# Kernel tuning notes

Hardware: AMD Instinct MI355X
Metric: run time of the kernel (lower is better)

## Reference

```python
import jax, jax.numpy as jnp
import numpy as np

NUM_ROUTERS = 8
K = 2
IN_DIM = 384
HID = 64
TEMP = 1.0
AUX_COEF = 0.05
EPS = 1e-12


def _l2norm(v, axis=-1):
    n = jnp.sqrt(jnp.sum(v * v, axis=axis, keepdims=True))
    return v / jnp.maximum(n, EPS)


def setup_inputs() -> dict:
    key = jax.random.key(0)
    ks = jax.random.split(key, 10)
    B, E = 8192, 1024
    s = 1.0 / np.sqrt(IN_DIM)
    return {
        "x": jax.random.normal(ks[0], (B, IN_DIM), jnp.float32),
        "reasoning_embeddings": jax.random.normal(ks[1], (E, IN_DIM), jnp.float32),
        "random_num": jax.random.uniform(ks[2], (B, 1), jnp.float32),
        "gate_w": jax.random.normal(ks[3], (IN_DIM, NUM_ROUTERS), jnp.float32) * s,
        "gate_b": jnp.zeros((NUM_ROUTERS,), jnp.float32),
        "Uw": jax.random.normal(ks[4], (NUM_ROUTERS, IN_DIM, HID), jnp.float32) * s,
        "Ub": jnp.zeros((NUM_ROUTERS, HID), jnp.float32),
        "Vw": jax.random.normal(ks[5], (NUM_ROUTERS, IN_DIM, HID), jnp.float32) * s,
        "Vb": jnp.zeros((NUM_ROUTERS, HID), jnp.float32),
    }


def reference(x, reasoning_embeddings, random_num, gate_w, gate_b, Uw, Ub, Vw, Vb):
    B = x.shape[0]
    # gate
    logits = x @ gate_w + gate_b                              # [B, R]
    probs = jax.nn.softmax(logits, axis=-1)
    topk_vals, topk_idxs = jax.lax.top_k(logits, K)           # [B, K]
    topk_mask = jax.nn.one_hot(topk_idxs, NUM_ROUTERS).sum(axis=1)  # [B, R]
    aux_loss = NUM_ROUTERS * (probs.mean(0) * topk_mask.mean(0)).sum() * AUX_COEF

    # all routers, batched (replaces the per-(i,j) python loop)
    xu = _l2norm(jnp.einsum("bd,rdh->rbh", x, Uw) + Ub[:, None, :])          # [R, B, H]
    ev = _l2norm(jnp.einsum("ed,rdh->reh", reasoning_embeddings, Vw) + Vb[:, None, :])  # [R, E, H]
    scores = jnp.einsum("rbh,reh->rbe", xu, ev)               # [R, B, E]
    all_out = jax.nn.softmax(scores / TEMP, axis=-1)          # [R, B, E]

    # gather top-k experts per sample
    all_out_b = jnp.transpose(all_out, (1, 0, 2))             # [B, R, E]
    router_outputs = jnp.take_along_axis(all_out_b, topk_idxs[:, :, None], axis=1)  # [B, K, E]

    gate_weights = jax.nn.softmax(topk_vals, axis=-1)[:, :, None]  # [B, K, 1]
    rea_probs = jnp.sum(router_outputs * gate_weights, axis=1)     # [B, E]

    # categorical sampling via inverse-CDF
    scores_cumsum = jnp.cumsum(rea_probs, axis=1)
    selected_index = jnp.argmax((scores_cumsum > random_num).astype(jnp.float32), axis=1)  # [B]
    log_probs = jnp.log(rea_probs[jnp.arange(B), selected_index])[:, None]  # [B, 1]
    return selected_index, log_probs, aux_loss
```

## Files before the change

kernel.cpp:

```cpp
#include <hip/hip_runtime.h>
#include <math.h>

#define B 8192
#define E 1024
#define D 384
#define H 64
#define R 8
#define NCHUNK 16
#define CHUNK_E 64

#define WS_COUNTS   0u
#define WS_CURSORS  32u
#define WS_PS       64u
#define WS_TOP2     256u
#define WS_GW       65792u
#define WS_LIST     131328u
#define WS_EVN      196864u
#define WS_XUN      2294016u
#define WS_C        6488320u
#define WS_POSMAP   7536896u

__global__ __launch_bounds__(256) void k_gate(
    const float* __restrict__ x, const float* __restrict__ gate_w,
    const float* __restrict__ gate_b, int2* __restrict__ top2,
    float2* __restrict__ gwv, int* __restrict__ counts, float* __restrict__ ps)
{
  __shared__ __align__(16) float gwT[R * 388];
  __shared__ float psl[R];
  __shared__ int   cl[R];
  int tid = threadIdx.x;
  for (int idx = tid; idx < D * R; idx += 256) {
    int k = idx >> 3, r = idx & 7;
    gwT[r * 388 + k] = gate_w[idx];
  }
  if (tid < R) { psl[tid] = 0.f; cl[tid] = 0; }
  __syncthreads();

  int l = tid & 63;
  int r = tid & 7;
  int b = blockIdx.x * 32 + (tid >> 3);
  float acc = gate_b[r];
  const float4* x4 = (const float4*)(x + (size_t)b * D);
  const float*  gr = gwT + r * 388;
#pragma unroll 4
  for (int q = 0; q < 96; ++q) {
    float4 xv = x4[q];
    float4 gv = *(const float4*)&gr[q * 4];
    acc = fmaf(xv.x, gv.x, acc);
    acc = fmaf(xv.y, gv.y, acc);
    acc = fmaf(xv.z, gv.z, acc);
    acc = fmaf(xv.w, gv.w, acc);
  }
  float lv[R];
#pragma unroll
  for (int rr = 0; rr < R; ++rr) lv[rr] = __shfl(acc, (l & ~7) + rr);
  int i0 = 0; float v0 = lv[0];
#pragma unroll
  for (int rr = 1; rr < R; ++rr) if (lv[rr] > v0) { v0 = lv[rr]; i0 = rr; }
  int i1 = (i0 == 0) ? 1 : 0; float v1 = lv[i1];
#pragma unroll
  for (int rr = 0; rr < R; ++rr)
    if (rr != i0 && lv[rr] > v1) { v1 = lv[rr]; i1 = rr; }
  float se = 0.f;
#pragma unroll
  for (int rr = 0; rr < R; ++rr) se += expf(lv[rr] - v0);
  float p = expf(acc - v0) / se;
  if (r == 0) {
    float e10 = expf(v1 - v0);
    top2[b] = make_int2(i0, i1);
    gwv[b]  = make_float2(1.f / (1.f + e10), e10 / (1.f + e10));
  }
  float pa = p;
  int   ca = (r == i0 ? 1 : 0) + (r == i1 ? 1 : 0);
#pragma unroll
  for (int m = 8; m < 64; m <<= 1) {
    pa += __shfl_xor(pa, m);
    ca += __shfl_xor(ca, m);
  }
  if (l < 8) { atomicAdd(&psl[r], pa); atomicAdd(&cl[r], ca); }
  __syncthreads();
  if (tid < R) { atomicAdd(&ps[tid], psl[tid]); atomicAdd(&counts[tid], cl[tid]); }
}

__global__ __launch_bounds__(256) void k_scatter(
    const int2* __restrict__ top2, const int* __restrict__ counts,
    const float* __restrict__ ps, int* __restrict__ cursors,
    int* __restrict__ list, int2* __restrict__ posmap, float* __restrict__ out_aux)
{
  __shared__ int lc[R];
  __shared__ int lbase[R];
  __shared__ int offs[R];
  int tid = threadIdx.x;
  if (tid < R) { lc[tid] = 0; offs[tid] = min(counts[tid], B); }
  __syncthreads();
  if (tid == 0) {
    int o = 0;
    for (int r2 = 0; r2 < R; ++r2) { int c = offs[r2]; offs[r2] = o; o += c; }
  }
  __syncthreads();
  int b = min(blockIdx.x * 256 + tid, B - 1);
  int2 t = top2[b];
  t.x &= 7; t.y &= 7;
  int p0 = atomicAdd(&lc[t.x], 1);
  int p1 = atomicAdd(&lc[t.y], 1);
  __syncthreads();
  if (tid < R) lbase[tid] = atomicAdd(&cursors[tid], lc[tid]);
  __syncthreads();
  int i0 = min(offs[t.x] + lbase[t.x] + p0, 2 * B - 1);
  int i1 = min(offs[t.y] + lbase[t.y] + p1, 2 * B - 1);
  list[i0] = b * 2 + 0;
  list[i1] = b * 2 + 1;
  posmap[b] = make_int2(i0, i1);
  if (blockIdx.x == 0 && tid == 0) {
    float s = 0.f;
    for (int r2 = 0; r2 < R; ++r2)
      s += (ps[r2] / (float)B) * ((float)min(counts[r2], B) / (float)B);
    out_aux[0] = (float)R * s * 0.05f;
  }
}

__global__ __launch_bounds__(128) void k_proj(
    const float* __restrict__ re, const float* __restrict__ x,
    const float* __restrict__ Vw, const float* __restrict__ Vb,
    const float* __restrict__ Uw, const float* __restrict__ Ub,
    const int* __restrict__ list, const int* __restrict__ counts,
    float* __restrict__ evnT, float* __restrict__ xunP)
{
  __shared__ __align__(16) float At[64 * 32];
  __shared__ __align__(16) float Wt[64 * 64];
  __shared__ int cntL[R];
  int tid = threadIdx.x;
  int bid = blockIdx.x;
  if (tid < R) cntL[tid] = min(counts[tid], B);
  __syncthreads();

  bool isE = (bid < 256);
  int r, row0, n, base = 0;
  const float* Wsrc; const float* bias;
  if (isE) {
    r = bid >> 5; row0 = (bid & 31) * 32; n = 32;
    Wsrc = Vw + (size_t)r * D * H; bias = Vb + r * H;
  } else {
    int idx = bid - 256;
    r = idx >> 8; row0 = (idx & 255) * 32;
    int cnt = cntL[r];
    if (row0 >= cnt) return;
    n = min(32, cnt - row0);
    for (int rr = 0; rr < r; ++rr) base += cntL[rr];
    base += row0;
    Wsrc = Uw + (size_t)r * D * H; bias = Ub + r * H;
  }

  int rowS = tid & 31, kq = tid >> 5;
  const float4* Arow;
  if (isE) {
    Arow = (const float4*)re + (size_t)(row0 + rowS) * 96;
  } else {
    int g = list[min(base + min(rowS, n - 1), 2 * B - 1)] & (2 * B - 1);
    Arow = (const float4*)x + (size_t)(g >> 1) * 96;
  }
  const float4* W4 = (const float4*)Wsrc;

  int rg = tid >> 4;
  int hg = tid & 15;
  float4 bv = *(const float4*)(bias + hg * 4);
  float acc[4][4];
#pragma unroll
  for (int i = 0; i < 4; ++i) {
    acc[i][0] = bv.x; acc[i][1] = bv.y; acc[i][2] = bv.z; acc[i][3] = bv.w;
  }

  for (int kt = 0; kt < 6; ++kt) {
    __syncthreads();
#pragma unroll
    for (int q = 0; q < 4; ++q) {
      float4 v = Arow[kt * 16 + kq + 4 * q];
      int kb = (kq + 4 * q) * 4;
      At[(kb + 0) * 32 + rowS] = v.x;
      At[(kb + 1) * 32 + rowS] = v.y;
      At[(kb + 2) * 32 + rowS] = v.z;
      At[(kb + 3) * 32 + rowS] = v.w;
    }
#pragma unroll
    for (int q = 0; q < 8; ++q) {
      int idx2 = tid + 128 * q;
      int k = idx2 >> 4, h4 = idx2 & 15;
      *(float4*)&Wt[k * 64 + h4 * 4] = W4[(size_t)(kt * 64 + k) * 16 + h4];
    }
    __syncthreads();
#pragma unroll 8
    for (int k = 0; k < 64; ++k) {
      float4 a4 = *(const float4*)&At[k * 32 + rg * 4];
      float4 w4 = *(const float4*)&Wt[k * 64 + hg * 4];
      const float* ap = (const float*)&a4;
      const float* wp = (const float*)&w4;
#pragma unroll
      for (int i = 0; i < 4; ++i)
#pragma unroll
        for (int j = 0; j < 4; ++j) acc[i][j] = fmaf(ap[i], wp[j], acc[i][j]);
    }
  }

  float rn[4];
#pragma unroll
  for (int i = 0; i < 4; ++i) {
    float ss = 0.f;
#pragma unroll
    for (int j = 0; j < 4; ++j) ss = fmaf(acc[i][j], acc[i][j], ss);
#pragma unroll
    for (int m = 1; m < 16; m <<= 1) ss += __shfl_xor(ss, m);
    rn[i] = 1.f / fmaxf(sqrtf(ss), 1e-12f);
  }

  if (isE) {
#pragma unroll
    for (int j = 0; j < 4; ++j) {
      float4 o;
      o.x = acc[0][j] * rn[0]; o.y = acc[1][j] * rn[1];
      o.z = acc[2][j] * rn[2]; o.w = acc[3][j] * rn[3];
      *(float4*)(evnT + (size_t)(r * 64 + hg * 4 + j) * 1024 + row0 + rg * 4) = o;
    }
  } else {
#pragma unroll
    for (int i = 0; i < 4; ++i) {
      int row = rg * 4 + i;
      if (row < n) {
        float4 o;
        o.x = acc[i][0] * rn[i]; o.y = acc[i][1] * rn[i];
        o.z = acc[i][2] * rn[i]; o.w = acc[i][3] * rn[i];
        *(float4*)(xunP + (size_t)(base + row) * H + hg * 4) = o;
      }
    }
  }
}

__global__ __launch_bounds__(256) void k_pass1(
    const float* __restrict__ evnT, const float* __restrict__ xunP,
    const int* __restrict__ counts, float* __restrict__ C)
{
  __shared__ __align__(16) float Xt[64 * 128];
  __shared__ __align__(16) float Et[64 * 64];
  __shared__ int cntL[R];
  int tid = threadIdx.x;
  if (tid < R) cntL[tid] = min(counts[tid], B);
  __syncthreads();

  int bid = blockIdx.x;
  int et    = bid & 15;
  int stile = (bid >> 4) & 63;
  int r     = bid >> 10;
  int cnt = cntL[r];
  if (cnt <= 0 || stile * 128 >= cnt) return;
  int off = 0;
  for (int rr = 0; rr < r; ++rr) off += cntL[rr];
  off += stile * 128;
  int n = min(128, cnt - stile * 128);
  int ebase = et * 64;

  {
    int row = tid >> 1;
    int rc  = min(row, n - 1);
    const float4* src = (const float4*)(xunP + (size_t)(off + rc) * H);
    int hq0 = (tid & 1) * 8;
#pragma unroll
    for (int q = 0; q < 8; ++q) {
      float4 v = src[hq0 + q];
      int h = (hq0 + q) * 4;
      Xt[(h + 0) * 128 + row] = v.x;
      Xt[(h + 1) * 128 + row] = v.y;
      Xt[(h + 2) * 128 + row] = v.z;
      Xt[(h + 3) * 128 + row] = v.w;
    }
  }
  {
#pragma unroll
    for (int q = 0; q < 4; ++q) {
      int idx = tid + 256 * q;
      int h = idx >> 4, e4 = idx & 15;
      float4 v = *(const float4*)(evnT + (size_t)(r * 64 + h) * 1024 + ebase + e4 * 4);
      *(float4*)&Et[h * 64 + e4 * 4] = v;
    }
  }
  __syncthreads();

  int sg = tid >> 4, egr = tid & 15;
  float acc[8][4];
#pragma unroll
  for (int i = 0; i < 8; ++i)
#pragma unroll
    for (int j = 0; j < 4; ++j) acc[i][j] = 0.f;

#pragma unroll 4
  for (int k = 0; k < 64; ++k) {
    float4 xa = *(const float4*)&Xt[k * 128 + sg * 8];
    float4 xb = *(const float4*)&Xt[k * 128 + sg * 8 + 4];
    float4 ev = *(const float4*)&Et[k * 64 + egr * 4];
    const float* ep = (const float*)&ev;
    const float* pa = (const float*)&xa;
    const float* pb = (const float*)&xb;
#pragma unroll
    for (int i = 0; i < 4; ++i)
#pragma unroll
      for (int j = 0; j < 4; ++j) {
        acc[i][j]     = fmaf(pa[i], ep[j], acc[i][j]);
        acc[i + 4][j] = fmaf(pb[i], ep[j], acc[i + 4][j]);
      }
  }

#pragma unroll
  for (int i = 0; i < 8; ++i) {
    float v = expf(acc[i][0]) + expf(acc[i][1]) + expf(acc[i][2]) + expf(acc[i][3]);
#pragma unroll
    for (int m = 1; m < 16; m <<= 1) v += __shfl_xor(v, m);
    int s = sg * 8 + i;
    if (egr == 0 && s < n) C[(size_t)(off + s) * NCHUNK + et] = v;
  }
}

__global__ __launch_bounds__(256) void k_pass2(
    const float* __restrict__ evnT, const float* __restrict__ xunP,
    const float* __restrict__ C, const int2* __restrict__ top2,
    const int2* __restrict__ posmap, const float2* __restrict__ gwv,
    const float* __restrict__ rnd, float* __restrict__ out)
{
  int tid = threadIdx.x;
  int lane = tid & 63;
  int b = blockIdx.x * 4 + (tid >> 6);
  if (b >= B) return;
  int2 t2 = top2[b];
  t2.x &= 7; t2.y &= 7;
  int2 pm = posmap[b];
  pm.x &= (2 * B - 1); pm.y &= (2 * B - 1);
  float2 gw = gwv[b];
  float rv = rnd[b];

  const float4* C04 = (const float4*)(C + (size_t)pm.x * NCHUNK);
  const float4* C14 = (const float4*)(C + (size_t)pm.y * NCHUNK);
  float c0[NCHUNK], c1[NCHUNK];
#pragma unroll
  for (int q = 0; q < 4; ++q) {
    float4 v0 = C04[q], v1 = C14[q];
    c0[q*4+0]=v0.x; c0[q*4+1]=v0.y; c0[q*4+2]=v0.z; c0[q*4+3]=v0.w;
    c1[q*4+0]=v1.x; c1[q*4+1]=v1.y; c1[q*4+2]=v1.z; c1[q*4+3]=v1.w;
  }
  float S0 = 0.f, S1 = 0.f;
#pragma unroll
  for (int j = 0; j < NCHUNK; ++j) { S0 += c0[j]; S1 += c1[j]; }
  float a0 = gw.x / S0, a1 = gw.y / S1;
  int cstar = -1; float prefix = 0.f; float run = 0.f;
#pragma unroll
  for (int j = 0; j < NCHUNK; ++j) {
    float nrun = run + (c0[j] * a0 + c1[j] * a1);
    if (cstar < 0 && nrun > rv) { cstar = j; prefix = run; }
    run = nrun;
  }
  float rtgt = rv;
  if (cstar < 0) { cstar = 0; prefix = 0.f; rtgt = -1.0f; }

  float xu0 = xunP[(size_t)pm.x * H + lane];
  float xu1 = xunP[(size_t)pm.y * H + lane];
  const float* E0 = evnT + (size_t)t2.x * 64 * 1024 + cstar * CHUNK_E + lane;
  const float* E1 = evnT + (size_t)t2.y * 64 * 1024 + cstar * CHUNK_E + lane;
  float d0 = 0.f, d1 = 0.f;
#pragma unroll 16
  for (int h = 0; h < 64; ++h) {
    float w0 = __shfl(xu0, h);
    float w1 = __shfl(xu1, h);
    d0 = fmaf(E0[(size_t)h * 1024], w0, d0);
    d1 = fmaf(E1[(size_t)h * 1024], w1, d1);
  }
  float rea = expf(d0) * a0 + expf(d1) * a1;
  float sc = rea;
#pragma unroll
  for (int d = 1; d < 64; d <<= 1) {
    float o = __shfl_up(sc, d);
    if (lane >= d) sc += o;
  }
  float cum = prefix + sc;
  unsigned long long m2 = __ballot(cum > rtgt);
  int estar = (m2 == 0ull) ? 63 : (int)__builtin_ctzll(m2);
  float p = __shfl(rea, estar);
  if (lane == 0) {
    int sel = cstar * CHUNK_E + estar;
    out[b]     = (float)sel;
    out[B + b] = logf(p);
  }
}

extern "C" void kernel_launch(void* const* d_in, const int* in_sizes, int n_in,
                              void* d_out, int out_size, void* d_ws, size_t ws_size,
                              hipStream_t stream)
{
  (void)in_sizes; (void)n_in; (void)out_size; (void)ws_size;
  const float* x      = (const float*)d_in[0];
  const float* re     = (const float*)d_in[1];
  const float* rnd    = (const float*)d_in[2];
  const float* gate_w = (const float*)d_in[3];
  const float* gate_b = (const float*)d_in[4];
  const float* Uw     = (const float*)d_in[5];
  const float* Ub     = (const float*)d_in[6];
  const float* Vw     = (const float*)d_in[7];
  const float* Vb     = (const float*)d_in[8];
  char* ws = (char*)d_ws;
  int*    counts  = (int*)(ws + WS_COUNTS);
  int*    cursors = (int*)(ws + WS_CURSORS);
  float*  ps      = (float*)(ws + WS_PS);
  int2*   top2    = (int2*)(ws + WS_TOP2);
  float2* gwv     = (float2*)(ws + WS_GW);
  int*    list    = (int*)(ws + WS_LIST);
  float*  evnT    = (float*)(ws + WS_EVN);
  float*  xunP    = (float*)(ws + WS_XUN);
  float*  Cc      = (float*)(ws + WS_C);
  int2*   posmap  = (int2*)(ws + WS_POSMAP);
  float* out = (float*)d_out;

  hipMemsetAsync(ws, 0, 256, stream);
  k_gate   <<<256,  256, 0, stream>>>(x, gate_w, gate_b, top2, gwv, counts, ps);
  k_scatter<<<32,   256, 0, stream>>>(top2, counts, ps, cursors, list, posmap, out + 2 * B);
  k_proj   <<<2304, 128, 0, stream>>>(re, x, Vw, Vb, Uw, Ub, list, counts, evnT, xunP);
  k_pass1  <<<8192, 256, 0, stream>>>(evnT, xunP, counts, Cc);
  k_pass2  <<<2048, 256, 0, stream>>>(evnT, xunP, Cc, top2, posmap, gwv, rnd, out);
}
```

Baseline: 184.7 us.

## Rewrite projection with wave-level readlane GEMM and widen pass1 E tiles

The projection kernel drops its shared-memory tiles. Each wave now computes 8 rows by 64 hidden units, holding weights in registers and broadcasting inputs with readlane, which removes LDS traffic and barriers. Pass1 doubles its E tile to 128 columns (8x8 accumulators per thread), halving the number of blocks and the reloads of each X tile. Router segment offsets are padded to multiples of 8 and the workspace is relaid out. The trade is higher register pressure and uncoalesced per-row weight loads in the projection.

```diff
diff --git a/kernel.cpp b/kernel.cpp
--- a/kernel.cpp
+++ b/kernel.cpp
@@ -8,17 +8,18 @@
 #define R 8
 #define NCHUNK 16
 #define CHUNK_E 64
+#define NPOS 16448
 
 #define WS_COUNTS   0u
 #define WS_CURSORS  32u
 #define WS_PS       64u
 #define WS_TOP2     256u
 #define WS_GW       65792u
-#define WS_LIST     131328u
-#define WS_EVN      196864u
-#define WS_XUN      2294016u
-#define WS_C        6488320u
-#define WS_POSMAP   7536896u
+#define WS_POSMAP   131328u
+#define WS_LIST     196864u
+#define WS_EVN      262656u
+#define WS_XUN      2359808u
+#define WS_C        6570496u
 
 __global__ __launch_bounds__(256) void k_gate(
     const float* __restrict__ x, const float* __restrict__ gate_w,
@@ -91,11 +92,11 @@
   __shared__ int lbase[R];
   __shared__ int offs[R];
   int tid = threadIdx.x;
-  if (tid < R) { lc[tid] = 0; offs[tid] = min(counts[tid], B); }
+  if (tid < R) lc[tid] = 0;
   __syncthreads();
   if (tid == 0) {
     int o = 0;
-    for (int r2 = 0; r2 < R; ++r2) { int c = offs[r2]; offs[r2] = o; o += c; }
+    for (int r2 = 0; r2 < R; ++r2) { offs[r2] = o; o += (min(counts[r2], B) + 7) & ~7; }
   }
   __syncthreads();
   int b = min(blockIdx.x * 256 + tid, B - 1);
@@ -106,8 +107,8 @@
   __syncthreads();
   if (tid < R) lbase[tid] = atomicAdd(&cursors[tid], lc[tid]);
   __syncthreads();
-  int i0 = min(offs[t.x] + lbase[t.x] + p0, 2 * B - 1);
-  int i1 = min(offs[t.y] + lbase[t.y] + p1, 2 * B - 1);
+  int i0 = min(offs[t.x] + lbase[t.x] + p0, NPOS - 1);
+  int i1 = min(offs[t.y] + lbase[t.y] + p1, NPOS - 1);
   list[i0] = b * 2 + 0;
   list[i1] = b * 2 + 1;
   posmap[b] = make_int2(i0, i1);
@@ -119,118 +120,96 @@
   }
 }
 
-__global__ __launch_bounds__(128) void k_proj(
+__global__ __launch_bounds__(256) void k_proj(
     const float* __restrict__ re, const float* __restrict__ x,
     const float* __restrict__ Vw, const float* __restrict__ Vb,
     const float* __restrict__ Uw, const float* __restrict__ Ub,
     const int* __restrict__ list, const int* __restrict__ counts,
     float* __restrict__ evnT, float* __restrict__ xunP)
 {
-  __shared__ __align__(16) float At[64 * 32];
-  __shared__ __align__(16) float Wt[64 * 64];
-  __shared__ int cntL[R];
   int tid = threadIdx.x;
+  int lane = tid & 63;
+  int wv = tid >> 6;
   int bid = blockIdx.x;
-  if (tid < R) cntL[tid] = min(counts[tid], B);
-  __syncthreads();
 
   bool isE = (bid < 256);
-  int r, row0, n, base = 0;
-  const float* Wsrc; const float* bias;
+  int r, g, n = 32, base = 0;
+  const float *W, *bias;
   if (isE) {
-    r = bid >> 5; row0 = (bid & 31) * 32; n = 32;
-    Wsrc = Vw + (size_t)r * D * H; bias = Vb + r * H;
+    r = bid >> 5; g = bid & 31;
+    W = Vw + (size_t)r * (D * H); bias = Vb + r * H;
   } else {
     int idx = bid - 256;
-    r = idx >> 8; row0 = (idx & 255) * 32;
-    int cnt = cntL[r];
-    if (row0 >= cnt) return;
-    n = min(32, cnt - row0);
-    for (int rr = 0; rr < r; ++rr) base += cntL[rr];
-    base += row0;
-    Wsrc = Uw + (size_t)r * D * H; bias = Ub + r * H;
-  }
-
-  int rowS = tid & 31, kq = tid >> 5;
-  const float4* Arow;
+    r = idx >> 8; g = idx & 255;
+    int cnt = min(counts[r], B);
+    if (g * 32 >= cnt) return;
+    n = min(32, cnt - g * 32);
+    for (int rr = 0; rr < r; ++rr) base += (min(counts[rr], B) + 7) & ~7;
+    base += g * 32;
+    W = Uw + (size_t)r * (D * H); bias = Ub + r * H;
+  }
+  int row0 = wv * 8;
+  if (row0 >= n) return;
+
+  const float* arow[8];
+#pragma unroll
+  for (int i = 0; i < 8; ++i) {
+    int rr = min(row0 + i, n - 1);
+    if (isE) {
+      arow[i] = re + (size_t)(g * 32 + rr) * D;
+    } else {
+      int gl = list[min(base + rr, NPOS - 1)];
+      gl = min(max(gl, 0), 2 * B - 1);
+      arow[i] = x + (size_t)(gl >> 1) * D;
+    }
+  }
+  float bv = bias[lane];
+  float acc[8];
+#pragma unroll
+  for (int i = 0; i < 8; ++i) acc[i] = bv;
+
+  for (int c = 0; c < 6; ++c) {
+    float w[64];
+#pragma unroll
+    for (int k = 0; k < 64; ++k) w[k] = W[(size_t)(c * 64 + k) * H + lane];
+    float xa[8];
+#pragma unroll
+    for (int i = 0; i < 8; ++i) xa[i] = arow[i][c * 64 + lane];
+#pragma unroll
+    for (int k = 0; k < 64; ++k) {
+      float wk = w[k];
+#pragma unroll
+      for (int i = 0; i < 8; ++i) {
+        float s = __uint_as_float(__builtin_amdgcn_readlane(__float_as_uint(xa[i]), k));
+        acc[i] = fmaf(s, wk, acc[i]);
+      }
+    }
+  }
+
+  float rn[8];
+#pragma unroll
+  for (int i = 0; i < 8; ++i) {
+    float ss = acc[i] * acc[i];
+#pragma unroll
+    for (int m = 1; m < 64; m <<= 1) ss += __shfl_xor(ss, m);
+    rn[i] = 1.f / fmaxf(sqrtf(ss), 1e-12f);
+  }
+
   if (isE) {
-    Arow = (const float4*)re + (size_t)(row0 + rowS) * 96;
+    int e0 = g * 32 + row0;
+    float4 o0, o1;
+    o0.x = acc[0] * rn[0]; o0.y = acc[1] * rn[1];
+    o0.z = acc[2] * rn[2]; o0.w = acc[3] * rn[3];
+    o1.x = acc[4] * rn[4]; o1.y = acc[5] * rn[5];
+    o1.z = acc[6] * rn[6]; o1.w = acc[7] * rn[7];
+    float* dst = evnT + (size_t)(r * 64 + lane) * 1024 + e0;
+    *(float4*)dst = o0;
+    *(float4*)(dst + 4) = o1;
   } else {
-    int g = list[min(base + min(rowS, n - 1), 2 * B - 1)] & (2 * B - 1);
-    Arow = (const float4*)x + (size_t)(g >> 1) * 96;
-  }
-  const float4* W4 = (const float4*)Wsrc;
-
-  int rg = tid >> 4;
-  int hg = tid & 15;
-  float4 bv = *(const float4*)(bias + hg * 4);
-  float acc[4][4];
-#pragma unroll
-  for (int i = 0; i < 4; ++i) {
-    acc[i][0] = bv.x; acc[i][1] = bv.y; acc[i][2] = bv.z; acc[i][3] = bv.w;
-  }
-
-  for (int kt = 0; kt < 6; ++kt) {
-    __syncthreads();
-#pragma unroll
-    for (int q = 0; q < 4; ++q) {
-      float4 v = Arow[kt * 16 + kq + 4 * q];
-      int kb = (kq + 4 * q) * 4;
-      At[(kb + 0) * 32 + rowS] = v.x;
-      At[(kb + 1) * 32 + rowS] = v.y;
-      At[(kb + 2) * 32 + rowS] = v.z;
-      At[(kb + 3) * 32 + rowS] = v.w;
-    }
-#pragma unroll
-    for (int q = 0; q < 8; ++q) {
-      int idx2 = tid + 128 * q;
-      int k = idx2 >> 4, h4 = idx2 & 15;
-      *(float4*)&Wt[k * 64 + h4 * 4] = W4[(size_t)(kt * 64 + k) * 16 + h4];
-    }
-    __syncthreads();
-#pragma unroll 8
-    for (int k = 0; k < 64; ++k) {
-      float4 a4 = *(const float4*)&At[k * 32 + rg * 4];
-      float4 w4 = *(const float4*)&Wt[k * 64 + hg * 4];
-      const float* ap = (const float*)&a4;
-      const float* wp = (const float*)&w4;
-#pragma unroll
-      for (int i = 0; i < 4; ++i)
-#pragma unroll
-        for (int j = 0; j < 4; ++j) acc[i][j] = fmaf(ap[i], wp[j], acc[i][j]);
-    }
-  }
-
-  float rn[4];
-#pragma unroll
-  for (int i = 0; i < 4; ++i) {
-    float ss = 0.f;
-#pragma unroll
-    for (int j = 0; j < 4; ++j) ss = fmaf(acc[i][j], acc[i][j], ss);
-#pragma unroll
-    for (int m = 1; m < 16; m <<= 1) ss += __shfl_xor(ss, m);
-    rn[i] = 1.f / fmaxf(sqrtf(ss), 1e-12f);
-  }
-
-  if (isE) {
-#pragma unroll
-    for (int j = 0; j < 4; ++j) {
-      float4 o;
-      o.x = acc[0][j] * rn[0]; o.y = acc[1][j] * rn[1];
-      o.z = acc[2][j] * rn[2]; o.w = acc[3][j] * rn[3];
-      *(float4*)(evnT + (size_t)(r * 64 + hg * 4 + j) * 1024 + row0 + rg * 4) = o;
-    }
-  } else {
-#pragma unroll
-    for (int i = 0; i < 4; ++i) {
-      int row = rg * 4 + i;
-      if (row < n) {
-        float4 o;
-        o.x = acc[i][0] * rn[i]; o.y = acc[i][1] * rn[i];
-        o.z = acc[i][2] * rn[i]; o.w = acc[i][3] * rn[i];
-        *(float4*)(xunP + (size_t)(base + row) * H + hg * 4) = o;
-      }
-    }
+#pragma unroll
+    for (int i = 0; i < 8; ++i)
+      if (row0 + i < n)
+        xunP[(size_t)(base + row0 + i) * H + lane] = acc[i] * rn[i];
   }
 }
 
@@ -239,23 +218,23 @@
     const int* __restrict__ counts, float* __restrict__ C)
 {
   __shared__ __align__(16) float Xt[64 * 128];
-  __shared__ __align__(16) float Et[64 * 64];
+  __shared__ __align__(16) float Et[64 * 128];
   __shared__ int cntL[R];
   int tid = threadIdx.x;
   if (tid < R) cntL[tid] = min(counts[tid], B);
   __syncthreads();
 
   int bid = blockIdx.x;
-  int et    = bid & 15;
-  int stile = (bid >> 4) & 63;
-  int r     = bid >> 10;
+  int et    = bid & 7;
+  int stile = (bid >> 3) & 63;
+  int r     = bid >> 9;
   int cnt = cntL[r];
   if (cnt <= 0 || stile * 128 >= cnt) return;
   int off = 0;
-  for (int rr = 0; rr < r; ++rr) off += cntL[rr];
+  for (int rr = 0; rr < r; ++rr) off += (cntL[rr] + 7) & ~7;
   off += stile * 128;
   int n = min(128, cnt - stile * 128);
-  int ebase = et * 64;
+  int ebase = et * 128;
 
   {
     int row = tid >> 1;
@@ -274,46 +253,57 @@
   }
   {
 #pragma unroll
-    for (int q = 0; q < 4; ++q) {
+    for (int q = 0; q < 8; ++q) {
       int idx = tid + 256 * q;
-      int h = idx >> 4, e4 = idx & 15;
+      int h = idx >> 5, e4 = idx & 31;
       float4 v = *(const float4*)(evnT + (size_t)(r * 64 + h) * 1024 + ebase + e4 * 4);
-      *(float4*)&Et[h * 64 + e4 * 4] = v;
+      *(float4*)&Et[h * 128 + e4 * 4] = v;
     }
   }
   __syncthreads();
 
   int sg = tid >> 4, egr = tid & 15;
-  float acc[8][4];
+  float acc[8][8];
 #pragma unroll
   for (int i = 0; i < 8; ++i)
 #pragma unroll
-    for (int j = 0; j < 4; ++j) acc[i][j] = 0.f;
+    for (int j = 0; j < 8; ++j) acc[i][j] = 0.f;
 
 #pragma unroll 4
   for (int k = 0; k < 64; ++k) {
     float4 xa = *(const float4*)&Xt[k * 128 + sg * 8];
     float4 xb = *(const float4*)&Xt[k * 128 + sg * 8 + 4];
-    float4 ev = *(const float4*)&Et[k * 64 + egr * 4];
-    const float* ep = (const float*)&ev;
+    float4 ea = *(const float4*)&Et[k * 128 + egr * 4];
+    float4 eb = *(const float4*)&Et[k * 128 + 64 + egr * 4];
     const float* pa = (const float*)&xa;
     const float* pb = (const float*)&xb;
+    const float* qa = (const float*)&ea;
+    const float* qb = (const float*)&eb;
 #pragma unroll
     for (int i = 0; i < 4; ++i)
 #pragma unroll
       for (int j = 0; j < 4; ++j) {
-        acc[i][j]     = fmaf(pa[i], ep[j], acc[i][j]);
-        acc[i + 4][j] = fmaf(pb[i], ep[j], acc[i + 4][j]);
+        acc[i][j]         = fmaf(pa[i], qa[j], acc[i][j]);
+        acc[i][j + 4]     = fmaf(pa[i], qb[j], acc[i][j + 4]);
+        acc[i + 4][j]     = fmaf(pb[i], qa[j], acc[i + 4][j]);
+        acc[i + 4][j + 4] = fmaf(pb[i], qb[j], acc[i + 4][j + 4]);
       }
   }
 
 #pragma unroll
   for (int i = 0; i < 8; ++i) {
-    float v = expf(acc[i][0]) + expf(acc[i][1]) + expf(acc[i][2]) + expf(acc[i][3]);
-#pragma unroll
-    for (int m = 1; m < 16; m <<= 1) v += __shfl_xor(v, m);
+    float cA = expf(acc[i][0]) + expf(acc[i][1]) + expf(acc[i][2]) + expf(acc[i][3]);
+    float cB = expf(acc[i][4]) + expf(acc[i][5]) + expf(acc[i][6]) + expf(acc[i][7]);
+#pragma unroll
+    for (int m = 1; m < 16; m <<= 1) {
+      cA += __shfl_xor(cA, m);
+      cB += __shfl_xor(cB, m);
+    }
     int s = sg * 8 + i;
-    if (egr == 0 && s < n) C[(size_t)(off + s) * NCHUNK + et] = v;
+    if (egr == 0 && s < n) {
+      C[(size_t)(off + s) * NCHUNK + et * 2]     = cA;
+      C[(size_t)(off + s) * NCHUNK + et * 2 + 1] = cB;
+    }
   }
 }
 
@@ -330,7 +320,8 @@
   int2 t2 = top2[b];
   t2.x &= 7; t2.y &= 7;
   int2 pm = posmap[b];
-  pm.x &= (2 * B - 1); pm.y &= (2 * B - 1);
+  pm.x = min(max(pm.x, 0), NPOS - 1);
+  pm.y = min(max(pm.y, 0), NPOS - 1);
   float2 gw = gwv[b];
   float rv = rnd[b];
 
@@ -407,17 +398,17 @@
   float*  ps      = (float*)(ws + WS_PS);
   int2*   top2    = (int2*)(ws + WS_TOP2);
   float2* gwv     = (float2*)(ws + WS_GW);
+  int2*   posmap  = (int2*)(ws + WS_POSMAP);
   int*    list    = (int*)(ws + WS_LIST);
   float*  evnT    = (float*)(ws + WS_EVN);
   float*  xunP    = (float*)(ws + WS_XUN);
   float*  Cc      = (float*)(ws + WS_C);
-  int2*   posmap  = (int2*)(ws + WS_POSMAP);
   float* out = (float*)d_out;
 
   hipMemsetAsync(ws, 0, 256, stream);
   k_gate   <<<256,  256, 0, stream>>>(x, gate_w, gate_b, top2, gwv, counts, ps);
   k_scatter<<<32,   256, 0, stream>>>(top2, counts, ps, cursors, list, posmap, out + 2 * B);
-  k_proj   <<<2304, 128, 0, stream>>>(re, x, Vw, Vb, Uw, Ub, list, counts, evnT, xunP);
-  k_pass1  <<<8192, 256, 0, stream>>>(evnT, xunP, counts, Cc);
+  k_proj   <<<2304, 256, 0, stream>>>(re, x, Vw, Vb, Uw, Ub, list, counts, evnT, xunP);
+  k_pass1  <<<4096, 256, 0, stream>>>(evnT, xunP, counts, Cc);
   k_pass2  <<<2048, 256, 0, stream>>>(evnT, xunP, Cc, top2, posmap, gwv, rnd, out);
 }
```

After: 212.7 us. 1.15x slower.
